# Performance work log

Hardware: AMD Instinct MI355X
Metric: run time of the kernel (lower is better)

The kernel has to match this reference:

```python
import jax, jax.numpy as jnp
import numpy as np

NUM_SLOTS = 8
SLOT_DIM = 64
HIDDEN_DIM = 128  # max(slot_dim, 128)
ITERS = 3
EPS = 1e-08
LN_EPS = 1e-05


def _ln(x, w, b):
    mu = jnp.mean(x, axis=-1, keepdims=True)
    var = jnp.mean(jnp.square(x - mu), axis=-1, keepdims=True)
    return (x - mu) * jax.lax.rsqrt(var + LN_EPS) * w + b


def setup_inputs() -> dict:
    key = jax.random.key(0)
    ks = jax.random.split(key, 16)
    b, n, d, h, n_s = 64, 4096, SLOT_DIM, HIDDEN_DIM, NUM_SLOTS
    s = 1.0 / np.sqrt(d)
    sh = 1.0 / np.sqrt(h)
    inp = {
        'inputs': jax.random.normal(ks[0], (b, n, d), jnp.float32),
        'mask': jax.random.randint(ks[1], (b, n), 0, 2, jnp.int32),
        'noise': jax.random.normal(ks[2], (b, n_s, d), jnp.float32),
        'slots_mu': jax.random.normal(ks[3], (1, 1, d), jnp.float32),
        'slots_sigma': jax.random.uniform(ks[4], (1, 1, d), jnp.float32),
        'Wq': jax.random.normal(ks[5], (d, d), jnp.float32) * s,
        'bq': jnp.zeros((d,), jnp.float32),
        'Wk': jax.random.normal(ks[6], (d, d), jnp.float32) * s,
        'bk': jnp.zeros((d,), jnp.float32),
        'Wv': jax.random.normal(ks[7], (d, d), jnp.float32) * s,
        'bv': jnp.zeros((d,), jnp.float32),
        'W_ih': jax.random.normal(ks[8], (3 * d, d), jnp.float32) * s,
        'b_ih': jnp.zeros((3 * d,), jnp.float32),
        'W_hh': jax.random.normal(ks[9], (3 * d, d), jnp.float32) * s,
        'b_hh': jnp.zeros((3 * d,), jnp.float32),
        'W1': jax.random.normal(ks[10], (h, d), jnp.float32) * s,
        'b1': jnp.zeros((h,), jnp.float32),
        'W2': jax.random.normal(ks[11], (d, h), jnp.float32) * sh,
        'b2': jnp.zeros((d,), jnp.float32),
        'ln_in_w': jnp.ones((d,), jnp.float32), 'ln_in_b': jnp.zeros((d,), jnp.float32),
        'ln_s_w': jnp.ones((d,), jnp.float32), 'ln_s_b': jnp.zeros((d,), jnp.float32),
        'ln_ff_w': jnp.ones((d,), jnp.float32), 'ln_ff_b': jnp.zeros((d,), jnp.float32),
    }
    return inp


def reference(inputs, mask, noise, slots_mu, slots_sigma, Wq, bq, Wk, bk, Wv, bv,
              W_ih, b_ih, W_hh, b_hh, W1, b1, W2, b2,
              ln_in_w, ln_in_b, ln_s_w, ln_s_b, ln_ff_w, ln_ff_b):
    b, n, d = inputs.shape
    scale = d ** (-0.5)
    # slots ~ Normal(mu, sigma) via reparameterization with fixed noise
    slots = slots_mu + slots_sigma * noise  # [b, n_s, d]
    m = (mask[:, :, None] != 0)  # [b, n, 1]
    x = _ln(inputs, ln_in_w, ln_in_b)
    k = x @ Wk.T + bk  # [b, n, d]
    v = x @ Wv.T + bv  # [b, n, d]
    for _ in range(ITERS):
        slots_prev = slots
        s_n = _ln(slots, ln_s_w, ln_s_b)
        q = s_n @ Wq.T + bq  # [b, n_s, d]
        dots = jnp.einsum('bid,bjd->bij', k, q) * scale  # [b, n, n_s]
        attn = jax.nn.softmax(dots, axis=-1) + EPS
        attn = jnp.where(m, attn, 0.0)
        attn = attn / jnp.sum(attn, axis=-2, keepdims=True)
        updates = jnp.einsum('bij,bid->bjd', attn, v)  # [b, n_s, d]
        # GRUCell(updates, slots_prev)
        gx = updates @ W_ih.T + b_ih  # [b, n_s, 3d]
        gh = slots_prev @ W_hh.T + b_hh
        xr, xz, xn = jnp.split(gx, 3, axis=-1)
        hr, hz, hn = jnp.split(gh, 3, axis=-1)
        r = jax.nn.sigmoid(xr + hr)
        z = jax.nn.sigmoid(xz + hz)
        nn_ = jnp.tanh(xn + r * hn)
        slots = (1.0 - z) * nn_ + z * slots_prev
        # residual MLP
        ff = _ln(slots, ln_ff_w, ln_ff_b)
        slots = slots + (jax.nn.relu(ff @ W1.T + b1) @ W2.T + b2)
    return slots
```

## Files before the change

kernel.cpp:

```cpp
#include <hip/hip_runtime.h>
#include <hip/hip_bf16.h>

typedef unsigned short u16;
typedef unsigned int u32;
typedef unsigned long long u64;

#define BB 64
#define NN 4096
#define DD 64
#define NSLOT 8
#define HH 128
#define NITER 3

#define BF16_ONES_PROBE 0x3F803F80u

#define OFF_BQ   53248
#define OFF_BK   53312
#define OFF_BV   53376
#define OFF_BIH  53440
#define OFF_BHH  53632
#define OFF_B1   53824
#define OFF_B2   53952
#define OFF_LIW  54016
#define OFF_LIB  54080
#define OFF_LSW  54144
#define OFF_LSB  54208
#define OFF_LFW  54272
#define OFF_LFB  54336
#define OFF_PK   58496

__device__ __forceinline__ float bf2f(u16 u) {
    union { u32 i; float f; } c; c.i = ((u32)u) << 16; return c.f;
}
__device__ __forceinline__ float bflo(u32 w) {
    union { u32 i; float f; } c; c.i = w << 16; return c.f;
}
__device__ __forceinline__ float bfhi(u32 w) {
    union { u32 i; float f; } c; c.i = w & 0xffff0000u; return c.f;
}
__device__ __forceinline__ u16 f2bf(float f) {
    __hip_bfloat16 h = __float2bfloat16(f);
    return *reinterpret_cast<u16*>(&h);
}
__device__ __forceinline__ float ldf(const void* p, int i, bool isbf) {
    return isbf ? bf2f(((const u16*)p)[i]) : ((const float*)p)[i];
}

__device__ __forceinline__ float wsum64(float x) {
    #pragma unroll
    for (int o = 32; o > 0; o >>= 1) x += __shfl_xor(x, o);
    return x;
}

__device__ __forceinline__ float ln64(float v, const float* __restrict__ g,
                                      const float* __restrict__ b, int lane) {
    float mu = wsum64(v) * (1.f / 64.f);
    float d = v - mu;
    float var = wsum64(d * d) * (1.f / 64.f);
    return d * rsqrtf(var + 1e-5f) * g[lane] + b[lane];
}

__device__ __forceinline__ float mat64q(const float* __restrict__ xs,
                                        const float* __restrict__ P,
                                        int lane, int wq) {
    const float4* p4 = (const float4*)P;
    const float4* x4 = (const float4*)xs;
    int c0 = wq << 2;
    float4 x0 = x4[c0], x1 = x4[c0 + 1], x2 = x4[c0 + 2], x3 = x4[c0 + 3];
    float4 w0 = p4[c0 * 64 + lane];
    float4 w1 = p4[(c0 + 1) * 64 + lane];
    float4 w2 = p4[(c0 + 2) * 64 + lane];
    float4 w3 = p4[(c0 + 3) * 64 + lane];
    float a0 = w0.x * x0.x + w0.y * x0.y + w0.z * x0.z + w0.w * x0.w;
    float a1 = w1.x * x1.x + w1.y * x1.y + w1.z * x1.z + w1.w * x1.w;
    float a2 = w2.x * x2.x + w2.y * x2.y + w2.z * x2.z + w2.w * x2.w;
    float a3 = w3.x * x3.x + w3.y * x3.y + w3.z * x3.z + w3.w * x3.w;
    return (a0 + a1) + (a2 + a3);
}

struct PrepArgs {
    const void* w[7];
    const void* v[13];
};

__global__ __launch_bounds__(256) void prep_w(PrepArgs a, float* __restrict__ wf,
                                              const u32* __restrict__ probe) {
    bool isbf = (*probe == BF16_ONES_PROBE);
    int idx = blockIdx.x * 256 + threadIdx.x;
    if (idx < 13 * 4096) {
        int blk = idx >> 12, r = idx & 4095;
        int c = r >> 8, rem = r & 255, j = rem >> 2, dd = rem & 3;
        int m = 4 * c + dd;
        float val;
        if      (blk == 0)  val = ldf(a.w[2], j * 64 + m, isbf);
        else if (blk == 1)  val = ldf(a.w[0], j * 64 + m, isbf);
        else if (blk == 2)  val = ldf(a.w[1], m * 64 + j, isbf);
        else if (blk < 6)   val = ldf(a.w[3], ((blk - 3) * 64 + j) * 64 + m, isbf);
        else if (blk < 9)   val = ldf(a.w[4], ((blk - 6) * 64 + j) * 64 + m, isbf);
        else if (blk < 11)  val = ldf(a.w[5], ((blk - 9) * 64 + j) * 64 + m, isbf);
        else                val = ldf(a.w[6], j * 128 + (blk - 11) * 64 + m, isbf);
        wf[OFF_PK + idx] = val;
    } else {
        int k = idx - 13 * 4096;
        const int voff[13] = {OFF_BQ, OFF_BK, OFF_BV, OFF_BIH, OFF_BHH, OFF_B1, OFF_B2,
                              OFF_LIW, OFF_LIB, OFF_LSW, OFF_LSB, OFF_LFW, OFF_LFB};
        const int vn[13]   = {64, 64, 64, 192, 192, 128, 64, 64, 64, 64, 64, 64, 64};
        #pragma unroll
        for (int t = 0; t < 13; t++) {
            if (k < vn[t]) { wf[voff[t] + k] = ldf(a.v[t], k, isbf); return; }
            k -= vn[t];
        }
    }
}

__device__ __forceinline__ void emit_qstate4(
        float qv, int b, int s, int bs, int lane, int wave,
        const float* __restrict__ wf, float* __restrict__ xa,
        float (*__restrict__ red)[64],
        float* __restrict__ gqp, float* __restrict__ Avec, float* __restrict__ Cvec) {
    if (wave == 0) xa[lane] = qv;
    __syncthreads();
    red[wave][lane] = mat64q(xa, wf + OFF_PK + 2 * 4096, lane, wave);
    __syncthreads();
    float qkv = red[0][lane] + red[1][lane] + red[2][lane] + red[3][lane];
    float gqv = wf[OFF_LIW + lane] * qkv;
    if (wave == 0) gqp[(b << 9) + (lane >> 2) * 32 + s * 4 + (lane & 3)] = gqv;
    float A  = wsum64(gqv);
    float bd = wsum64(qv * wf[OFF_BK + lane]);
    float cq = wsum64(wf[OFF_LIB + lane] * qkv);
    if (wave == 0 && lane == 0) { Avec[bs] = A; Cvec[bs] = cq + bd; }
}

__global__ __launch_bounds__(256, 1) void init_slots(
        const void* __restrict__ noise, const void* __restrict__ mu, const void* __restrict__ sg,
        const float* __restrict__ wf, float* __restrict__ slots,
        float* __restrict__ gqp, float* __restrict__ Avec, float* __restrict__ Cvec,
        float* __restrict__ acc1, float* __restrict__ ssv, float* __restrict__ A2v,
        const u32* __restrict__ probe) {
    __shared__ __align__(16) float xa[64];
    __shared__ float red[4][64];
    bool isbf = (*probe == BF16_ONES_PROBE);
    int bs = blockIdx.x;
    int b = bs >> 3, s = bs & 7;
    int tid = threadIdx.x, wave = tid >> 6, lane = tid & 63;
    int idx = bs * DD + lane;
    float sl = ldf(mu, lane, isbf) + ldf(sg, lane, isbf) * ldf(noise, idx, isbf);
    if (wave == 0) {
        slots[idx] = sl;
        acc1[idx] = 0.f;
        if (lane == 0) { ssv[bs] = 0.f; A2v[bs] = 0.f; }
    }
    float sn = ln64(sl, wf + OFF_LSW, wf + OFF_LSB, lane);
    if (wave == 0) xa[lane] = sn;
    __syncthreads();
    red[wave][lane] = mat64q(xa, wf + OFF_PK + 1 * 4096, lane, wave);
    __syncthreads();
    float qv = wf[OFF_BQ + lane] + red[0][lane] + red[1][lane] + red[2][lane] + red[3][lane];
    emit_qstate4(qv, b, s, bs, lane, wave, wf, xa, red, gqp, Avec, Cvec);
}

__global__ __launch_bounds__(256) void fused_attn(
        const void* __restrict__ xin, const int* __restrict__ mask,
        const float* __restrict__ gqp, const float* __restrict__ Avec,
        const float* __restrict__ Cvec,
        float* __restrict__ acc1, float* __restrict__ ssv, float* __restrict__ A2v,
        const u32* __restrict__ probe) {
    __shared__ float4 aw4[256][2];
    __shared__ float racc[4][NSLOT][64];
    __shared__ float rss[4][NSLOT];
    __shared__ float rA2[4][NSLOT];
    __shared__ u64 wmask[4];

    bool isbf = (*probe == BF16_ONES_PROBE);
    int b = blockIdx.x >> 4;
    int base = (blockIdx.x & 15) << 8;
    int tid = threadIdx.x;
    int wave = tid >> 6, lane = tid & 63;

    size_t gt = ((size_t)b << 12) + base + tid;
    int mk = mask[gt];
    const float4* gq4 = (const float4*)(gqp + ((size_t)b << 9));
    float sum = 0.f, sq = 0.f;
    float d[8] = {0.f, 0.f, 0.f, 0.f, 0.f, 0.f, 0.f, 0.f};
    if (isbf) {
        const uint4* xr = (const uint4*)((const u16*)xin + gt * 64);
        uint4 xrg[8];
        #pragma unroll
        for (int i = 0; i < 8; i++) xrg[i] = xr[i];
        #pragma unroll
        for (int c = 0; c < 16; c++) {
            u32 wa = (c & 1) ? xrg[c >> 1].z : xrg[c >> 1].x;
            u32 wb = (c & 1) ? xrg[c >> 1].w : xrg[c >> 1].y;
            float x0 = bflo(wa), x1 = bfhi(wa), x2 = bflo(wb), x3 = bfhi(wb);
            sum += x0 + x1 + x2 + x3;
            sq  += x0 * x0 + x1 * x1 + x2 * x2 + x3 * x3;
            #pragma unroll
            for (int s = 0; s < 8; s++) {
                float4 q = gq4[c * 8 + s];
                d[s] += q.x * x0 + q.y * x1 + q.z * x2 + q.w * x3;
            }
        }
    } else {
        const float4* xr = (const float4*)((const float*)xin + gt * 64);
        #pragma unroll
        for (int c = 0; c < 16; c++) {
            float4 xv = xr[c];
            sum += xv.x + xv.y + xv.z + xv.w;
            sq  += xv.x * xv.x + xv.y * xv.y + xv.z * xv.z + xv.w * xv.w;
            #pragma unroll
            for (int s = 0; s < 8; s++) {
                float4 q = gq4[c * 8 + s];
                d[s] += q.x * xv.x + q.y * xv.y + q.z * xv.z + q.w * xv.w;
            }
        }
    }
    float muv = sum * (1.f / 64.f);
    float var = sq * (1.f / 64.f) - muv * muv;
    float rs = rsqrtf(var + 1e-5f);
    const float* Av = Avec + (b << 3);
    const float* Cv = Cvec + (b << 3);
    #pragma unroll
    for (int s = 0; s < 8; s++)
        d[s] = 0.125f * (rs * d[s] - rs * muv * Av[s] + Cv[s]);

    float mx = d[0];
    #pragma unroll
    for (int s = 1; s < 8; s++) mx = fmaxf(mx, d[s]);
    float den = 0.f;
    #pragma unroll
    for (int s = 0; s < 8; s++) { d[s] = expf(d[s] - mx); den += d[s]; }
    float inv = 1.f / den;
    float attn[8], aw[8];
    #pragma unroll
    for (int s = 0; s < 8; s++) {
        attn[s] = (mk != 0) ? (d[s] * inv + 1e-8f) : 0.f;
        aw[s] = attn[s] * rs;
    }
    {
        float4 w0; w0.x = aw[0]; w0.y = aw[1]; w0.z = aw[2]; w0.w = aw[3];
        float4 w1; w1.x = aw[4]; w1.y = aw[5]; w1.z = aw[6]; w1.w = aw[7];
        aw4[tid][0] = w0; aw4[tid][1] = w1;
    }
    u64 bal = __ballot(mk != 0);
    if (lane == 0) wmask[wave] = bal;
    #pragma unroll
    for (int s = 0; s < 8; s++) {
        float t1 = wsum64(attn[s]);
        float t2 = wsum64(aw[s] * muv);
        if (lane == 0) { rss[wave][s] = t1; rA2[wave][s] = t2; }
    }
    __syncthreads();

    u64 bits = wmask[wave];
    float acc[8] = {0.f, 0.f, 0.f, 0.f, 0.f, 0.f, 0.f, 0.f};
    size_t rowbase = ((size_t)b << 12) + base + (wave << 6);
    const u16* xb16 = (const u16*)xin + rowbase * 64 + lane;
    const float* xf32 = (const float*)xin + rowbase * 64 + lane;
    #pragma unroll 8
    for (int t = 0; t < 64; t++) {
        if ((bits >> t) & 1ULL) {
            float xv = isbf ? bf2f(xb16[t * 64]) : xf32[t * 64];
            float4 a0 = aw4[(wave << 6) + t][0];
            float4 a1 = aw4[(wave << 6) + t][1];
            acc[0] += a0.x * xv; acc[1] += a0.y * xv;
            acc[2] += a0.z * xv; acc[3] += a0.w * xv;
            acc[4] += a1.x * xv; acc[5] += a1.y * xv;
            acc[6] += a1.z * xv; acc[7] += a1.w * xv;
        }
    }
    #pragma unroll
    for (int s = 0; s < 8; s++) racc[wave][s][lane] = acc[s];
    __syncthreads();
    if (wave == 0) {
        float* ag = acc1 + ((size_t)b << 9);
        #pragma unroll
        for (int s = 0; s < 8; s++) {
            float v = racc[0][s][lane] + racc[1][s][lane] + racc[2][s][lane] + racc[3][s][lane];
            atomicAdd(ag + s * 64 + lane, v);
        }
        if (lane < NSLOT) {
            float t1 = rss[0][lane] + rss[1][lane] + rss[2][lane] + rss[3][lane];
            float t2 = rA2[0][lane] + rA2[1][lane] + rA2[2][lane] + rA2[3][lane];
            atomicAdd(ssv + (b << 3) + lane, t1);
            atomicAdd(A2v + (b << 3) + lane, t2);
        }
    }
}

__global__ __launch_bounds__(256, 1) void finalize_k(
        const float* __restrict__ wf, float* __restrict__ acc1, float* __restrict__ ssv,
        float* __restrict__ A2v, float* __restrict__ slots,
        float* __restrict__ gqp, float* __restrict__ Avec, float* __restrict__ Cvec,
        void* __restrict__ out, int last, const u32* __restrict__ probe) {
    __shared__ __align__(16) float xa[64];
    __shared__ __align__(16) float xb[64];
    __shared__ float red[6][4][64];
    bool isbf = (*probe == BF16_ONES_PROBE);
    int bs = blockIdx.x;
    int b = bs >> 3, s = bs & 7;
    int tid = threadIdx.x, wave = tid >> 6, lane = tid & 63;
    int idx = bs * DD + lane;
    const float* P = wf + OFF_PK;

    float sm   = ssv[bs];
    float a2v_ = A2v[bs];
    float ac   = acc1[idx];
    float sp   = slots[idx];

    float un = wf[OFF_LIW + lane] * (ac - a2v_) / sm + wf[OFF_LIB + lane];
    if (wave == 0) xa[lane] = un;
    __syncthreads();
    if (wave == 0) {
        acc1[idx] = 0.f;
        if (lane == 0) { ssv[bs] = 0.f; A2v[bs] = 0.f; }
    }

    red[0][wave][lane] = mat64q(xa, P + 0 * 4096, lane, wave);
    __syncthreads();
    #define SUM4(k) (red[k][0][lane] + red[k][1][lane] + red[k][2][lane] + red[k][3][lane])
    float uv = wf[OFF_BV + lane] + SUM4(0);
    if (wave == 0) { xa[lane] = uv; xb[lane] = sp; }
    __syncthreads();

    red[0][wave][lane] = mat64q(xa, P + 3 * 4096, lane, wave);
    red[1][wave][lane] = mat64q(xa, P + 4 * 4096, lane, wave);
    red[2][wave][lane] = mat64q(xa, P + 5 * 4096, lane, wave);
    red[3][wave][lane] = mat64q(xb, P + 6 * 4096, lane, wave);
    red[4][wave][lane] = mat64q(xb, P + 7 * 4096, lane, wave);
    red[5][wave][lane] = mat64q(xb, P + 8 * 4096, lane, wave);
    __syncthreads();
    float gxr = wf[OFF_BIH + lane]       + SUM4(0);
    float gxz = wf[OFF_BIH + 64 + lane]  + SUM4(1);
    float gxn = wf[OFF_BIH + 128 + lane] + SUM4(2);
    float ghr = wf[OFF_BHH + lane]       + SUM4(3);
    float ghz = wf[OFF_BHH + 64 + lane]  + SUM4(4);
    float ghn = wf[OFF_BHH + 128 + lane] + SUM4(5);
    float r = 1.f / (1.f + expf(-(gxr + ghr)));
    float z = 1.f / (1.f + expf(-(gxz + ghz)));
    float nn = tanhf(gxn + r * ghn);
    float snew = (1.f - z) * nn + z * sp;

    float ff = ln64(snew, wf + OFF_LFW, wf + OFF_LFB, lane);
    if (wave == 0) xa[lane] = ff;
    __syncthreads();
    red[0][wave][lane] = mat64q(xa, P + 9 * 4096, lane, wave);
    red[1][wave][lane] = mat64q(xa, P + 10 * 4096, lane, wave);
    __syncthreads();
    float h1a = fmaxf(wf[OFF_B1 + lane] + SUM4(0), 0.f);
    float h1b = fmaxf(wf[OFF_B1 + 64 + lane] + SUM4(1), 0.f);
    if (wave == 0) { xa[lane] = h1a; xb[lane] = h1b; }
    __syncthreads();
    red[0][wave][lane] = mat64q(xa, P + 11 * 4096, lane, wave)
                       + mat64q(xb, P + 12 * 4096, lane, wave);
    __syncthreads();
    float o = snew + wf[OFF_B2 + lane] + SUM4(0);

    if (wave == 0) slots[idx] = o;
    if (last) {
        if (wave == 0) {
            if (isbf) ((u16*)out)[idx] = f2bf(o);
            else      ((float*)out)[idx] = o;
        }
    } else {
        float sn2 = ln64(o, wf + OFF_LSW, wf + OFF_LSB, lane);
        if (wave == 0) xa[lane] = sn2;
        __syncthreads();
        red[0][wave][lane] = mat64q(xa, P + 1 * 4096, lane, wave);
        __syncthreads();
        float qv = wf[OFF_BQ + lane] + SUM4(0);
        emit_qstate4(qv, b, s, bs, lane, wave, wf, xa, red[0], gqp, Avec, Cvec);
    }
    #undef SUM4
}

extern "C" void kernel_launch(void* const* d_in, const int* in_sizes, int n_in,
                              void* d_out, int out_size, void* d_ws, size_t ws_size,
                              hipStream_t stream) {
    const void* xin   = d_in[0];
    const int* mask   = (const int*)d_in[1];
    const void* noise = d_in[2];
    const void* mu    = d_in[3];
    const void* sg    = d_in[4];
    const u32* probe  = (const u32*)d_in[19];

    char* ws = (char*)d_ws;
    float* wf = (float*)ws;

    size_t o = 524288;
    float* gqp   = (float*)(ws + o); o += (size_t)BB * 512 * 4;
    float* Avec  = (float*)(ws + o); o += (size_t)BB * NSLOT * 4;
    float* Cvec  = (float*)(ws + o); o += (size_t)BB * NSLOT * 4;
    float* acc1  = (float*)(ws + o); o += (size_t)BB * NSLOT * DD * 4;
    float* ssv   = (float*)(ws + o); o += (size_t)BB * NSLOT * 4;
    float* A2v   = (float*)(ws + o); o += (size_t)BB * NSLOT * 4;
    float* slots = (float*)(ws + o); o += (size_t)BB * NSLOT * DD * 4;

    PrepArgs pa;
    pa.w[0] = d_in[5];
    pa.w[1] = d_in[7];
    pa.w[2] = d_in[9];
    pa.w[3] = d_in[11];
    pa.w[4] = d_in[13];
    pa.w[5] = d_in[15];
    pa.w[6] = d_in[17];
    static const int vidx[13] = {6, 8, 10, 12, 14, 16, 18, 19, 20, 21, 22, 23, 24};
    for (int j = 0; j < 13; j++) pa.v[j] = d_in[vidx[j]];

    prep_w<<<213, 256, 0, stream>>>(pa, wf, probe);
    init_slots<<<BB * NSLOT, 256, 0, stream>>>(noise, mu, sg, wf, slots,
                                               gqp, Avec, Cvec, acc1, ssv, A2v, probe);

    for (int it = 0; it < NITER; it++) {
        fused_attn<<<BB * 16, 256, 0, stream>>>(xin, mask, gqp, Avec, Cvec,
                                                acc1, ssv, A2v, probe);
        finalize_k<<<BB * NSLOT, 256, 0, stream>>>(wf, acc1, ssv, A2v, slots,
                                                   gqp, Avec, Cvec,
                                                   d_out, it == NITER - 1 ? 1 : 0, probe);
    }
}
```

Measured before the change: 291.3 us.

## Split each token's dot products across two threads and skip masked tokens

Each block now covers 128 tokens instead of 256. Two threads share one token, each handling half of the 64 feature dimensions; their partial dot products and LN statistics are combined through shared memory, and the attention-weighted accumulation runs over 32 rows per wave. The grid is doubled, which gives more parallelism and fewer registers' worth of work per thread. Masked-out tokens now skip the input load and dot-product work entirely. The cost is an extra barrier and shared-memory exchange, idle threads during the softmax stage, and twice as many atomic adds into the accumulators.

```diff
diff --git a/kernel.cpp b/kernel.cpp
--- a/kernel.cpp
+++ b/kernel.cpp
@@ -165,103 +165,122 @@
         const float* __restrict__ Cvec,
         float* __restrict__ acc1, float* __restrict__ ssv, float* __restrict__ A2v,
         const u32* __restrict__ probe) {
-    __shared__ float4 aw4[256][2];
-    __shared__ float racc[4][NSLOT][64];
-    __shared__ float rss[4][NSLOT];
-    __shared__ float rA2[4][NSLOT];
-    __shared__ u64 wmask[4];
+    __shared__ float shbuf[2048];
+    __shared__ float4 aw4[128][2];
+    __shared__ float rss[2][NSLOT];
+    __shared__ float rA2[2][NSLOT];
+    __shared__ u64 wmask[2];
 
     bool isbf = (*probe == BF16_ONES_PROBE);
-    int b = blockIdx.x >> 4;
-    int base = (blockIdx.x & 15) << 8;
+    int b = blockIdx.x >> 5;
+    int base = (blockIdx.x & 31) << 7;
     int tid = threadIdx.x;
     int wave = tid >> 6, lane = tid & 63;
-
-    size_t gt = ((size_t)b << 12) + base + tid;
+    int k = tid & 127, half = tid >> 7;
+
+    size_t gt = ((size_t)b << 12) + base + k;
     int mk = mask[gt];
     const float4* gq4 = (const float4*)(gqp + ((size_t)b << 9));
     float sum = 0.f, sq = 0.f;
     float d[8] = {0.f, 0.f, 0.f, 0.f, 0.f, 0.f, 0.f, 0.f};
-    if (isbf) {
-        const uint4* xr = (const uint4*)((const u16*)xin + gt * 64);
-        uint4 xrg[8];
-        #pragma unroll
-        for (int i = 0; i < 8; i++) xrg[i] = xr[i];
-        #pragma unroll
-        for (int c = 0; c < 16; c++) {
-            u32 wa = (c & 1) ? xrg[c >> 1].z : xrg[c >> 1].x;
-            u32 wb = (c & 1) ? xrg[c >> 1].w : xrg[c >> 1].y;
-            float x0 = bflo(wa), x1 = bfhi(wa), x2 = bflo(wb), x3 = bfhi(wb);
-            sum += x0 + x1 + x2 + x3;
-            sq  += x0 * x0 + x1 * x1 + x2 * x2 + x3 * x3;
+    if (mk) {
+        if (isbf) {
+            const uint4* xr = (const uint4*)((const u16*)xin + gt * 64) + (half << 2);
+            uint4 xrg[4];
             #pragma unroll
-            for (int s = 0; s < 8; s++) {
-                float4 q = gq4[c * 8 + s];
-                d[s] += q.x * x0 + q.y * x1 + q.z * x2 + q.w * x3;
+            for (int i = 0; i < 4; i++) xrg[i] = xr[i];
+            #pragma unroll
+            for (int j = 0; j < 8; j++) {
+                int c = (half << 3) + j;
+                u32 wa = (j & 1) ? xrg[j >> 1].z : xrg[j >> 1].x;
+                u32 wb = (j & 1) ? xrg[j >> 1].w : xrg[j >> 1].y;
+                float x0 = bflo(wa), x1 = bfhi(wa), x2 = bflo(wb), x3 = bfhi(wb);
+                sum += x0 + x1 + x2 + x3;
+                sq  += x0 * x0 + x1 * x1 + x2 * x2 + x3 * x3;
+                #pragma unroll
+                for (int s = 0; s < 8; s++) {
+                    float4 q = gq4[c * 8 + s];
+                    d[s] += q.x * x0 + q.y * x1 + q.z * x2 + q.w * x3;
+                }
             }
-        }
-    } else {
-        const float4* xr = (const float4*)((const float*)xin + gt * 64);
-        #pragma unroll
-        for (int c = 0; c < 16; c++) {
-            float4 xv = xr[c];
-            sum += xv.x + xv.y + xv.z + xv.w;
-            sq  += xv.x * xv.x + xv.y * xv.y + xv.z * xv.z + xv.w * xv.w;
+        } else {
+            const float4* xr = (const float4*)((const float*)xin + gt * 64) + (half << 3);
             #pragma unroll
-            for (int s = 0; s < 8; s++) {
-                float4 q = gq4[c * 8 + s];
-                d[s] += q.x * xv.x + q.y * xv.y + q.z * xv.z + q.w * xv.w;
+            for (int j = 0; j < 8; j++) {
+                float4 xv = xr[j];
+                int c = (half << 3) + j;
+                sum += xv.x + xv.y + xv.z + xv.w;
+                sq  += xv.x * xv.x + xv.y * xv.y + xv.z * xv.z + xv.w * xv.w;
+                #pragma unroll
+                for (int s = 0; s < 8; s++) {
+                    float4 q = gq4[c * 8 + s];
+                    d[s] += q.x * xv.x + q.y * xv.y + q.z * xv.z + q.w * xv.w;
+                }
             }
         }
     }
-    float muv = sum * (1.f / 64.f);
-    float var = sq * (1.f / 64.f) - muv * muv;
-    float rs = rsqrtf(var + 1e-5f);
-    const float* Av = Avec + (b << 3);
-    const float* Cv = Cvec + (b << 3);
-    #pragma unroll
-    for (int s = 0; s < 8; s++)
-        d[s] = 0.125f * (rs * d[s] - rs * muv * Av[s] + Cv[s]);
-
-    float mx = d[0];
-    #pragma unroll
-    for (int s = 1; s < 8; s++) mx = fmaxf(mx, d[s]);
-    float den = 0.f;
-    #pragma unroll
-    for (int s = 0; s < 8; s++) { d[s] = expf(d[s] - mx); den += d[s]; }
-    float inv = 1.f / den;
-    float attn[8], aw[8];
-    #pragma unroll
-    for (int s = 0; s < 8; s++) {
-        attn[s] = (mk != 0) ? (d[s] * inv + 1e-8f) : 0.f;
-        aw[s] = attn[s] * rs;
-    }
-    {
+    float (*comb)[12] = (float (*)[12])shbuf;
+    if (half) {
+        #pragma unroll
+        for (int s = 0; s < 8; s++) comb[k][s] = d[s];
+        comb[k][8] = sum; comb[k][9] = sq;
+    }
+    __syncthreads();
+    if (half == 0) {
+        #pragma unroll
+        for (int s = 0; s < 8; s++) d[s] += comb[k][s];
+        sum += comb[k][8]; sq += comb[k][9];
+
+        float muv = sum * (1.f / 64.f);
+        float var = sq * (1.f / 64.f) - muv * muv;
+        float rs = rsqrtf(var + 1e-5f);
+        const float* Av = Avec + (b << 3);
+        const float* Cv = Cvec + (b << 3);
+        #pragma unroll
+        for (int s = 0; s < 8; s++)
+            d[s] = 0.125f * (rs * d[s] - rs * muv * Av[s] + Cv[s]);
+
+        float mx = d[0];
+        #pragma unroll
+        for (int s = 1; s < 8; s++) mx = fmaxf(mx, d[s]);
+        float den = 0.f;
+        #pragma unroll
+        for (int s = 0; s < 8; s++) { d[s] = expf(d[s] - mx); den += d[s]; }
+        float inv = 1.f / den;
+        float attn[8], aw[8];
+        #pragma unroll
+        for (int s = 0; s < 8; s++) {
+            attn[s] = (mk != 0) ? (d[s] * inv + 1e-8f) : 0.f;
+            aw[s] = attn[s] * rs;
+        }
         float4 w0; w0.x = aw[0]; w0.y = aw[1]; w0.z = aw[2]; w0.w = aw[3];
         float4 w1; w1.x = aw[4]; w1.y = aw[5]; w1.z = aw[6]; w1.w = aw[7];
-        aw4[tid][0] = w0; aw4[tid][1] = w1;
-    }
-    u64 bal = __ballot(mk != 0);
-    if (lane == 0) wmask[wave] = bal;
-    #pragma unroll
-    for (int s = 0; s < 8; s++) {
-        float t1 = wsum64(attn[s]);
-        float t2 = wsum64(aw[s] * muv);
-        if (lane == 0) { rss[wave][s] = t1; rA2[wave][s] = t2; }
-    }
-    __syncthreads();
-
-    u64 bits = wmask[wave];
+        aw4[k][0] = w0; aw4[k][1] = w1;
+
+        u64 bal = __ballot(mk != 0);
+        if (lane == 0) wmask[wave] = bal;
+        #pragma unroll
+        for (int s = 0; s < 8; s++) {
+            float t1 = wsum64(attn[s]);
+            float t2 = wsum64(aw[s] * muv);
+            if (lane == 0) { rss[wave][s] = t1; rA2[wave][s] = t2; }
+        }
+    }
+    __syncthreads();
+
+    float (*racc)[NSLOT][64] = (float (*)[NSLOT][64])shbuf;
+    u32 bits = (u32)(wmask[wave >> 1] >> ((wave & 1) << 5));
     float acc[8] = {0.f, 0.f, 0.f, 0.f, 0.f, 0.f, 0.f, 0.f};
-    size_t rowbase = ((size_t)b << 12) + base + (wave << 6);
+    size_t rowbase = ((size_t)b << 12) + base + (wave << 5);
     const u16* xb16 = (const u16*)xin + rowbase * 64 + lane;
     const float* xf32 = (const float*)xin + rowbase * 64 + lane;
+    int awbase = wave << 5;
     #pragma unroll 8
-    for (int t = 0; t < 64; t++) {
-        if ((bits >> t) & 1ULL) {
+    for (int t = 0; t < 32; t++) {
+        if ((bits >> t) & 1u) {
             float xv = isbf ? bf2f(xb16[t * 64]) : xf32[t * 64];
-            float4 a0 = aw4[(wave << 6) + t][0];
-            float4 a1 = aw4[(wave << 6) + t][1];
+            float4 a0 = aw4[awbase + t][0];
+            float4 a1 = aw4[awbase + t][1];
             acc[0] += a0.x * xv; acc[1] += a0.y * xv;
             acc[2] += a0.z * xv; acc[3] += a0.w * xv;
             acc[4] += a1.x * xv; acc[5] += a1.y * xv;
@@ -279,8 +298,8 @@
             atomicAdd(ag + s * 64 + lane, v);
         }
         if (lane < NSLOT) {
-            float t1 = rss[0][lane] + rss[1][lane] + rss[2][lane] + rss[3][lane];
-            float t2 = rA2[0][lane] + rA2[1][lane] + rA2[2][lane] + rA2[3][lane];
+            float t1 = rss[0][lane] + rss[1][lane];
+            float t2 = rA2[0][lane] + rA2[1][lane];
             atomicAdd(ssv + (b << 3) + lane, t1);
             atomicAdd(A2v + (b << 3) + lane, t2);
         }
@@ -411,7 +430,7 @@
                                                gqp, Avec, Cvec, acc1, ssv, A2v, probe);
 
     for (int it = 0; it < NITER; it++) {
-        fused_attn<<<BB * 16, 256, 0, stream>>>(xin, mask, gqp, Avec, Cvec,
+        fused_attn<<<BB * 32, 256, 0, stream>>>(xin, mask, gqp, Avec, Cvec,
                                                 acc1, ssv, A2v, probe);
         finalize_k<<<BB * NSLOT, 256, 0, stream>>>(wf, acc1, ssv, A2v, slots,
                                                    gqp, Avec, Cvec,
```

Result: no change. 285.8 us (-1.9%).

## Stage bf16 input rows in LDS and skip loads for masked tokens

Applied to the files above, without the earlier changes.

In the bf16 path, each thread copies its input row into shared memory, so the second weighted-sum pass reads x from LDS instead of reloading it from global memory. Masked-out tokens now skip the row load and the LN/dot computation entirely. The per-wave slot-sum reductions are atomically added straight from each wave instead of going through shared arrays and wave 0. This adds about 40 KB of shared memory, which may lower occupancy, plus an extra barrier and four times as many atomics on the sum buffers.

```diff
diff --git a/kernel.cpp b/kernel.cpp
--- a/kernel.cpp
+++ b/kernel.cpp
@@ -165,11 +165,10 @@
         const float* __restrict__ Cvec,
         float* __restrict__ acc1, float* __restrict__ ssv, float* __restrict__ A2v,
         const u32* __restrict__ probe) {
-    __shared__ float4 aw4[256][2];
-    __shared__ float racc[4][NSLOT][64];
-    __shared__ float rss[4][NSLOT];
-    __shared__ float rA2[4][NSLOT];
-    __shared__ u64 wmask[4];
+    __shared__ __align__(16) char shb[40960];
+    u16 (*xs)[DD]           = reinterpret_cast<u16(*)[DD]>(shb);
+    float (*racc)[NSLOT][64] = reinterpret_cast<float(*)[NSLOT][64]>(shb);
+    float4 (*aw4)[2]         = reinterpret_cast<float4(*)[2]>(shb + 32768);
 
     bool isbf = (*probe == BF16_ONES_PROBE);
     int b = blockIdx.x >> 4;
@@ -183,34 +182,44 @@
     float sum = 0.f, sq = 0.f;
     float d[8] = {0.f, 0.f, 0.f, 0.f, 0.f, 0.f, 0.f, 0.f};
     if (isbf) {
-        const uint4* xr = (const uint4*)((const u16*)xin + gt * 64);
-        uint4 xrg[8];
-        #pragma unroll
-        for (int i = 0; i < 8; i++) xrg[i] = xr[i];
-        #pragma unroll
-        for (int c = 0; c < 16; c++) {
-            u32 wa = (c & 1) ? xrg[c >> 1].z : xrg[c >> 1].x;
-            u32 wb = (c & 1) ? xrg[c >> 1].w : xrg[c >> 1].y;
-            float x0 = bflo(wa), x1 = bfhi(wa), x2 = bflo(wb), x3 = bfhi(wb);
-            sum += x0 + x1 + x2 + x3;
-            sq  += x0 * x0 + x1 * x1 + x2 * x2 + x3 * x3;
+        if (mk) {
+            const uint4* xr = (const uint4*)((const u16*)xin + gt * 64);
+            uint4 xrg[8];
             #pragma unroll
-            for (int s = 0; s < 8; s++) {
-                float4 q = gq4[c * 8 + s];
-                d[s] += q.x * x0 + q.y * x1 + q.z * x2 + q.w * x3;
+            for (int i = 0; i < 8; i++) xrg[i] = xr[i];
+            uint2* xrow = (uint2*)&xs[tid][0];
+            #pragma unroll
+            for (int i = 0; i < 8; i++) {
+                xrow[2 * i]     = make_uint2(xrg[i].x, xrg[i].y);
+                xrow[2 * i + 1] = make_uint2(xrg[i].z, xrg[i].w);
             }
+            #pragma unroll
+            for (int c = 0; c < 16; c++) {
+                u32 wa = (c & 1) ? xrg[c >> 1].z : xrg[c >> 1].x;
+                u32 wb = (c & 1) ? xrg[c >> 1].w : xrg[c >> 1].y;
+                float x0 = bflo(wa), x1 = bfhi(wa), x2 = bflo(wb), x3 = bfhi(wb);
+                sum += x0 + x1 + x2 + x3;
+                sq  += x0 * x0 + x1 * x1 + x2 * x2 + x3 * x3;
+                #pragma unroll
+                for (int s = 0; s < 8; s++) {
+                    float4 q = gq4[c * 8 + s];
+                    d[s] += q.x * x0 + q.y * x1 + q.z * x2 + q.w * x3;
+                }
+            }
         }
     } else {
-        const float4* xr = (const float4*)((const float*)xin + gt * 64);
-        #pragma unroll
-        for (int c = 0; c < 16; c++) {
-            float4 xv = xr[c];
-            sum += xv.x + xv.y + xv.z + xv.w;
-            sq  += xv.x * xv.x + xv.y * xv.y + xv.z * xv.z + xv.w * xv.w;
+        if (mk) {
+            const float4* xr = (const float4*)((const float*)xin + gt * 64);
             #pragma unroll
-            for (int s = 0; s < 8; s++) {
-                float4 q = gq4[c * 8 + s];
-                d[s] += q.x * xv.x + q.y * xv.y + q.z * xv.z + q.w * xv.w;
+            for (int c = 0; c < 16; c++) {
+                float4 xv = xr[c];
+                sum += xv.x + xv.y + xv.z + xv.w;
+                sq  += xv.x * xv.x + xv.y * xv.y + xv.z * xv.z + xv.w * xv.w;
+                #pragma unroll
+                for (int s = 0; s < 8; s++) {
+                    float4 q = gq4[c * 8 + s];
+                    d[s] += q.x * xv.x + q.y * xv.y + q.z * xv.z + q.w * xv.w;
+                }
             }
         }
     }
@@ -242,32 +251,53 @@
         aw4[tid][0] = w0; aw4[tid][1] = w1;
     }
     u64 bal = __ballot(mk != 0);
-    if (lane == 0) wmask[wave] = bal;
+    float t1[8], t2[8];
     #pragma unroll
     for (int s = 0; s < 8; s++) {
-        float t1 = wsum64(attn[s]);
-        float t2 = wsum64(aw[s] * muv);
-        if (lane == 0) { rss[wave][s] = t1; rA2[wave][s] = t2; }
-    }
-    __syncthreads();
-
-    u64 bits = wmask[wave];
+        t1[s] = wsum64(attn[s]);
+        t2[s] = wsum64(aw[s] * muv);
+    }
+    if (lane == 0) {
+        #pragma unroll
+        for (int s = 0; s < 8; s++) {
+            atomicAdd(ssv + (b << 3) + s, t1[s]);
+            atomicAdd(A2v + (b << 3) + s, t2[s]);
+        }
+    }
+    __syncthreads();
+
     float acc[8] = {0.f, 0.f, 0.f, 0.f, 0.f, 0.f, 0.f, 0.f};
-    size_t rowbase = ((size_t)b << 12) + base + (wave << 6);
-    const u16* xb16 = (const u16*)xin + rowbase * 64 + lane;
-    const float* xf32 = (const float*)xin + rowbase * 64 + lane;
-    #pragma unroll 8
-    for (int t = 0; t < 64; t++) {
-        if ((bits >> t) & 1ULL) {
-            float xv = isbf ? bf2f(xb16[t * 64]) : xf32[t * 64];
-            float4 a0 = aw4[(wave << 6) + t][0];
-            float4 a1 = aw4[(wave << 6) + t][1];
-            acc[0] += a0.x * xv; acc[1] += a0.y * xv;
-            acc[2] += a0.z * xv; acc[3] += a0.w * xv;
-            acc[4] += a1.x * xv; acc[5] += a1.y * xv;
-            acc[6] += a1.z * xv; acc[7] += a1.w * xv;
-        }
-    }
+    int tb = wave << 6;
+    if (isbf) {
+        #pragma unroll 8
+        for (int t = 0; t < 64; t++) {
+            if ((bal >> t) & 1ULL) {
+                float xv = bf2f(xs[tb + t][lane]);
+                float4 a0 = aw4[tb + t][0];
+                float4 a1 = aw4[tb + t][1];
+                acc[0] += a0.x * xv; acc[1] += a0.y * xv;
+                acc[2] += a0.z * xv; acc[3] += a0.w * xv;
+                acc[4] += a1.x * xv; acc[5] += a1.y * xv;
+                acc[6] += a1.z * xv; acc[7] += a1.w * xv;
+            }
+        }
+    } else {
+        size_t rowbase = ((size_t)b << 12) + base + tb;
+        const float* xf32 = (const float*)xin + rowbase * 64 + lane;
+        #pragma unroll 8
+        for (int t = 0; t < 64; t++) {
+            if ((bal >> t) & 1ULL) {
+                float xv = xf32[t * 64];
+                float4 a0 = aw4[tb + t][0];
+                float4 a1 = aw4[tb + t][1];
+                acc[0] += a0.x * xv; acc[1] += a0.y * xv;
+                acc[2] += a0.z * xv; acc[3] += a0.w * xv;
+                acc[4] += a1.x * xv; acc[5] += a1.y * xv;
+                acc[6] += a1.z * xv; acc[7] += a1.w * xv;
+            }
+        }
+    }
+    __syncthreads();
     #pragma unroll
     for (int s = 0; s < 8; s++) racc[wave][s][lane] = acc[s];
     __syncthreads();
@@ -277,12 +307,6 @@
         for (int s = 0; s < 8; s++) {
             float v = racc[0][s][lane] + racc[1][s][lane] + racc[2][s][lane] + racc[3][s][lane];
             atomicAdd(ag + s * 64 + lane, v);
-        }
-        if (lane < NSLOT) {
-            float t1 = rss[0][lane] + rss[1][lane] + rss[2][lane] + rss[3][lane];
-            float t2 = rA2[0][lane] + rA2[1][lane] + rA2[2][lane] + rA2[3][lane];
-            atomicAdd(ssv + (b << 3) + lane, t1);
-            atomicAdd(A2v + (b << 3) + lane, t2);
         }
     }
 }
```

New measurement: 375.1 us. +28.7%, slower.
